# Optimization experiments

Hardware: AMD Instinct MI355X
Metric: run time of the kernel (lower is better)

Reference implementation:

```python
import jax, jax.numpy as jnp
import numpy as np

B, D, V, T = 256, 1024, 32000, 64  # num_seqs, hidden dim, vocab, history len


def setup_inputs() -> dict:
    key = jax.random.key(0)
    ks = jax.random.split(key, 8)
    hidden = jax.random.normal(ks[0], (B, D), dtype=jnp.float32)
    embedding = jax.random.normal(ks[1], (V, D), dtype=jnp.float32) * (1.0 / np.sqrt(D))
    output_tokens = jax.random.randint(ks[2], (B, T), 0, V, dtype=jnp.int64)
    presence_penalties = jax.random.uniform(ks[3], (B,), dtype=jnp.float32)
    frequency_penalties = jax.random.uniform(ks[4], (B,), dtype=jnp.float32)
    temperatures = jax.random.uniform(ks[5], (B,), dtype=jnp.float32) + 0.5  # > eps
    top_ps = jax.random.uniform(ks[6], (B,), dtype=jnp.float32) * 0.5 + 0.5  # in [0.5, 1.0)
    top_ks = jax.random.randint(ks[7], (B,), 1, V, dtype=jnp.int64)
    return {
        "hidden": hidden,
        "embedding": embedding,
        "output_tokens": output_tokens,
        "presence_penalties": presence_penalties,
        "frequency_penalties": frequency_penalties,
        "temperatures": temperatures,
        "top_ps": top_ps,
        "top_ks": top_ks,
    }


def reference(hidden, embedding, output_tokens, presence_penalties,
              frequency_penalties, temperatures, top_ps, top_ks):
    # 1) logits = pruned hidden states @ embedding^T  -> [B, V]
    logits = jnp.einsum("bd,vd->bv", hidden, embedding)
    b, v = logits.shape

    # 2) presence/frequency penalties via per-row token histogram (np.bincount equiv)
    rows = jnp.broadcast_to(jnp.arange(b)[:, None], output_tokens.shape)
    counts = jnp.zeros((b, v), logits.dtype).at[rows, output_tokens].add(1.0)
    logits = logits - frequency_penalties[:, None] * counts \
                    - presence_penalties[:, None] * (counts > 0).astype(logits.dtype)

    # 3) temperature scaling
    logits = logits / temperatures[:, None]

    # 4) probabilities
    probs = jax.nn.softmax(logits, axis=-1)

    # 5) top-p / top-k: descending sort, cumsum masks, scatter back via inverse perm
    order = jnp.argsort(-probs, axis=-1)                       # descending order
    probs_sort = jnp.take_along_axis(probs, order, axis=-1)
    probs_cum = jnp.cumsum(probs_sort, axis=-1)
    top_p_mask = (probs_cum - probs_sort) > top_ps[:, None]
    top_k_mask = jnp.arange(v)[None, :] >= top_ks[:, None]
    probs_sort = jnp.where(top_p_mask | top_k_mask, 0.0, probs_sort)
    inv = jnp.argsort(order, axis=-1)
    filtered_probs = jnp.take_along_axis(probs_sort, inv, axis=-1)  # original order
    return filtered_probs
```

## Files before the change

### kernel.cpp

```cpp
#include <hip/hip_runtime.h>
#include <math.h>

#define NB 256
#define NV 32000
#define ND 1024
#define NT 64

#define GN 64
#define BSTR 40
#define NKB 64
#define AKBF 8192
#define NGBLK (NV / GN)
#define INV2048F 4.8828125e-4f

#define NBIN 1024
#define HSTR 1032
#define HTOT (4 * HSTR)
#define FIX2 4294967296.0
#define SMASK ((1ull << 48) - 1ull)
#define SMEM_BYTES (NV * 4 + HTOT * 4)

typedef _Float16 f16x8 __attribute__((ext_vector_type(8)));
typedef _Float16 f16x4 __attribute__((ext_vector_type(4)));
typedef float f32x16 __attribute__((ext_vector_type(16)));

struct RowP2 {
  unsigned long long basePack;
  unsigned long long toppZfix;
  unsigned pfx;
  int ktop;
  float invZ;
  unsigned ustar;
  int m;
  int cEq;
};

__device__ __forceinline__ unsigned mono_enc(float f) {
  unsigned u = __float_as_uint(f);
  return (u & 0x80000000u) ? ~u : (u | 0x80000000u);
}
__device__ __forceinline__ float mono_dec(unsigned u) {
  return (u & 0x80000000u) ? __uint_as_float(u & 0x7FFFFFFFu) : __uint_as_float(~u);
}

__global__ __launch_bounds__(256) void convert_A(const float* __restrict__ hidden,
                                                 _Float16* __restrict__ A3) {
  const int g = blockIdx.x * 256 + threadIdx.x;
  const int kb = g >> 10, rem = g & 1023, r = rem >> 2, c = rem & 3;
  const float4 a4 = *(const float4*)(hidden + (size_t)r * ND + kb * 16 + c * 4);
  const float v[4] = {a4.x, a4.y, a4.z, a4.w};
  f16x4 h4, q4;
#pragma unroll
  for (int q = 0; q < 4; q++) {
    const _Float16 hh = (_Float16)v[q];
    h4[q] = hh;
    q4[q] = (_Float16)((v[q] - (float)hh) * 2048.0f);
  }
  const int s = r >> 5, l31 = r & 31;
  const int lh = c >> 1, j4 = (c & 1) * 4;
  const int lane = l31 + (lh << 5);
  _Float16* base = A3 + (size_t)kb * AKBF;
  *(f16x4*)(base + ((s * 2 + 0) * 64 + lane) * 8 + j4) = h4;
  *(f16x4*)(base + ((s * 2 + 1) * 64 + lane) * 8 + j4) = q4;
}

__global__ __launch_bounds__(256, 2) void gemm_f16s(
    const float* __restrict__ Bm, const _Float16* __restrict__ A3,
    const float* __restrict__ temp, unsigned* __restrict__ rowmax,
    float* __restrict__ C) {
  __shared__ _Float16 Bls[2][GN * BSTR];
  __shared__ float s_invT[256];
  __shared__ unsigned s_pm[256];

  const int t = threadIdx.x;
  const int l = t & 63, w = t >> 6;
  const int n0 = blockIdx.x * GN;
  s_invT[t] = 1.0f / temp[t];
  s_pm[t] = 0u;

  f32x16 accH[2][2] = {};
  f32x16 accC[2][2] = {};

  const int bn = t >> 2, bk4 = (t & 3) * 4;
  const int l31 = l & 31, lh = l >> 5;
  const int ka = lh * 8;
  const int mb = w * 64;

  const float* browp = Bm + (size_t)(n0 + bn) * ND + bk4;
  const _Float16* aB = A3 + 2048 * w + l * 8;

  f16x8 eh0, eh1, eq0, eq1;
  f16x8 oh0, oh1, oq0, oq1;

#define LOADA(P, KB)                                                  \
  do {                                                                \
    const _Float16* ap_ = aB + (size_t)(KB) * AKBF;                   \
    P##h0 = *(const f16x8*)(ap_);                                     \
    P##q0 = *(const f16x8*)(ap_ + 512);                               \
    P##h1 = *(const f16x8*)(ap_ + 1024);                              \
    P##q1 = *(const f16x8*)(ap_ + 1536);                              \
  } while (0)

#define BCONV(BV, DST)                                                \
  do {                                                                \
    f16x4 h4_, q4_;                                                   \
    const float vv_[4] = {(BV).x, (BV).y, (BV).z, (BV).w};            \
    _Pragma("unroll") for (int j_ = 0; j_ < 4; j_++) {                \
      const _Float16 h_ = (_Float16)vv_[j_];                          \
      h4_[j_] = h_;                                                   \
      q4_[j_] = (_Float16)((vv_[j_] - (float)h_) * 2048.0f);          \
    }                                                                 \
    _Float16* prow_ = (DST) + bn * BSTR;                              \
    *(f16x4*)(prow_ + bk4) = h4_;                                     \
    *(f16x4*)(prow_ + 16 + bk4) = q4_;                                \
  } while (0)

#define COMPUTE(P, CUR)                                                                     \
  do {                                                                                      \
    const _Float16* Bp_ = &Bls[CUR][0] + (size_t)l31 * BSTR + ka;                           \
    f16x8 b0h_ = *(const f16x8*)(Bp_);                                                      \
    f16x8 b1h_ = *(const f16x8*)(Bp_ + 32 * BSTR);                                          \
    accH[0][0] = __builtin_amdgcn_mfma_f32_32x32x16_f16(P##h0, b0h_, accH[0][0], 0, 0, 0);  \
    accH[0][1] = __builtin_amdgcn_mfma_f32_32x32x16_f16(P##h0, b1h_, accH[0][1], 0, 0, 0);  \
    accH[1][0] = __builtin_amdgcn_mfma_f32_32x32x16_f16(P##h1, b0h_, accH[1][0], 0, 0, 0);  \
    accH[1][1] = __builtin_amdgcn_mfma_f32_32x32x16_f16(P##h1, b1h_, accH[1][1], 0, 0, 0);  \
    f16x8 b0q_ = *(const f16x8*)(Bp_ + 16);                                                 \
    f16x8 b1q_ = *(const f16x8*)(Bp_ + 32 * BSTR + 16);                                     \
    accC[0][0] = __builtin_amdgcn_mfma_f32_32x32x16_f16(P##h0, b0q_, accC[0][0], 0, 0, 0);  \
    accC[0][1] = __builtin_amdgcn_mfma_f32_32x32x16_f16(P##h0, b1q_, accC[0][1], 0, 0, 0);  \
    accC[1][0] = __builtin_amdgcn_mfma_f32_32x32x16_f16(P##h1, b0q_, accC[1][0], 0, 0, 0);  \
    accC[1][1] = __builtin_amdgcn_mfma_f32_32x32x16_f16(P##h1, b1q_, accC[1][1], 0, 0, 0);  \
    accC[0][0] = __builtin_amdgcn_mfma_f32_32x32x16_f16(P##q0, b0h_, accC[0][0], 0, 0, 0);  \
    accC[0][1] = __builtin_amdgcn_mfma_f32_32x32x16_f16(P##q0, b1h_, accC[0][1], 0, 0, 0);  \
    accC[1][0] = __builtin_amdgcn_mfma_f32_32x32x16_f16(P##q1, b0h_, accC[1][0], 0, 0, 0);  \
    accC[1][1] = __builtin_amdgcn_mfma_f32_32x32x16_f16(P##q1, b1h_, accC[1][1], 0, 0, 0);  \
  } while (0)

  LOADA(e, 0);
  __builtin_amdgcn_sched_barrier(0);
  float4 bv0 = *(const float4*)(browp);
  __builtin_amdgcn_sched_barrier(0);
  LOADA(o, 1);
  __builtin_amdgcn_sched_barrier(0);
  float4 bvA = *(const float4*)(browp + 16);
  __builtin_amdgcn_sched_barrier(0);
  BCONV(bv0, &Bls[0][0]);
  asm volatile("s_waitcnt lgkmcnt(0)\ns_barrier" ::: "memory");

  float4 bvB;
  for (int kb = 0; kb < 62; kb += 2) {
    COMPUTE(e, 0);
    __builtin_amdgcn_sched_barrier(0);
    LOADA(e, kb + 2);
    __builtin_amdgcn_sched_barrier(0);
    bvB = *(const float4*)(browp + (size_t)(kb + 2) * 16);
    __builtin_amdgcn_sched_barrier(0);
    BCONV(bvA, &Bls[1][0]);
    asm volatile("s_waitcnt lgkmcnt(0)\ns_barrier" ::: "memory");

    COMPUTE(o, 1);
    __builtin_amdgcn_sched_barrier(0);
    LOADA(o, kb + 3);
    __builtin_amdgcn_sched_barrier(0);
    bvA = *(const float4*)(browp + (size_t)(kb + 3) * 16);
    __builtin_amdgcn_sched_barrier(0);
    BCONV(bvB, &Bls[0][0]);
    asm volatile("s_waitcnt lgkmcnt(0)\ns_barrier" ::: "memory");
  }
  COMPUTE(e, 0);
  __builtin_amdgcn_sched_barrier(0);
  BCONV(bvA, &Bls[1][0]);
  asm volatile("s_waitcnt lgkmcnt(0)\ns_barrier" ::: "memory");
  COMPUTE(o, 1);

#undef LOADA
#undef BCONV
#undef COMPUTE

#pragma unroll
  for (int mi = 0; mi < 2; mi++) {
#pragma unroll
    for (int r = 0; r < 16; r++) {
      const int row = mb + mi * 32 + (r & 3) + 8 * (r >> 2) + 4 * lh;
      const float it = s_invT[row];
      float v0 = (accH[mi][0][r] + accC[mi][0][r] * INV2048F) * it;
      float v1 = (accH[mi][1][r] + accC[mi][1][r] * INV2048F) * it;
      C[(size_t)row * NV + n0 + l31] = v0;
      C[(size_t)row * NV + n0 + 32 + l31] = v1;
      float mx = fmaxf(v0, v1);
#pragma unroll
      for (int o = 1; o < 32; o <<= 1) mx = fmaxf(mx, __shfl_xor(mx, o));
      if (l31 == 0) atomicMax(&s_pm[row], mono_enc(mx));
    }
  }
  __syncthreads();
  atomicMax(&rowmax[t], s_pm[t]);
}

__global__ __launch_bounds__(1024) void sample_row(
    float* __restrict__ buf, const unsigned* __restrict__ rowmax,
    const int* __restrict__ toks, const float* __restrict__ pres,
    const float* __restrict__ freq, const float* __restrict__ temp,
    const float* __restrict__ topp_a, const int* __restrict__ topk_a) {
  extern __shared__ char smem[];
  float* e = (float*)smem;
  unsigned* hist = (unsigned*)(smem + NV * 4);
  unsigned long long* suf = (unsigned long long*)hist;
  __shared__ int s_tok[NT];
  __shared__ int s_bs;
  __shared__ RowP2 sp;

  const int b = blockIdx.x, t = threadIdx.x;
  const int cp = (t >> 6) & 1;
  unsigned* loP = hist + cp * HSTR;
  unsigned* hcP = hist + 2 * HSTR + cp * HSTR;
  float* row = buf + (size_t)b * NV;

#define HACC(EV, BIN)                                                    \
  do {                                                                   \
    unsigned long long f_ = (unsigned long long)((double)(EV) * FIX2);   \
    unsigned flo_ = (unsigned)f_;                                        \
    unsigned old_ = atomicAdd(&loP[BIN], flo_);                          \
    unsigned hc_ = 0x10000u + (unsigned)(f_ >> 32) +                     \
                   ((old_ + flo_ < flo_) ? 1u : 0u);                     \
    atomicAdd(&hcP[BIN], hc_);                                           \
  } while (0)

  if (t < NT) s_tok[t] = toks[b * NT + t];
  for (int i = t; i < HTOT; i += 1024) hist[i] = 0u;
  for (int i4 = t; i4 < NV / 4; i4 += 1024)
    *(float4*)(e + i4 * 4) = *(const float4*)(row + i4 * 4);
  __syncthreads();

  if (t < NT) {
    const int tk = s_tok[t];
    bool first = true; int cnt = 0;
    for (int j = 0; j < NT; j++)
      if (s_tok[j] == tk) { if (j < t) first = false; cnt++; }
    if (first) e[tk] -= (freq[b] * (float)cnt + pres[b]) / temp[b];
  }
  __syncthreads();

  const float M = mono_dec(rowmax[b]);
  for (int i4 = t; i4 < NV / 4; i4 += 1024) {
    float4 x4 = *(const float4*)(e + i4 * 4);
    float4 e4;
    e4.x = expf(x4.x - M); e4.y = expf(x4.y - M);
    e4.z = expf(x4.z - M); e4.w = expf(x4.w - M);
    *(float4*)(e + i4 * 4) = e4;
    unsigned k;
    k = __float_as_uint(e4.x); if (k) HACC(e4.x, k >> 20);
    k = __float_as_uint(e4.y); if (k) HACC(e4.y, k >> 20);
    k = __float_as_uint(e4.z); if (k) HACC(e4.z, k >> 20);
    k = __float_as_uint(e4.w); if (k) HACC(e4.w, k >> 20);
  }
  __syncthreads();

  for (int level = 0; level < 3; level++) {
    const unsigned lo0 = hist[t], lo1 = hist[HSTR + t];
    const unsigned hc0 = hist[2 * HSTR + t], hc1 = hist[3 * HSTR + t];
    const unsigned c = (hc0 >> 16) + (hc1 >> 16);
    const unsigned long long sum =
        (((unsigned long long)((hc0 & 0xFFFFu) + (hc1 & 0xFFFFu))) << 32) +
        (unsigned long long)lo0 + (unsigned long long)lo1;
    const unsigned long long v = ((unsigned long long)c << 48) + sum;
    __syncthreads();
    suf[t] = v;
    __syncthreads();
    for (int off = 1; off < NBIN; off <<= 1) {
      unsigned long long add = (t + off < NBIN) ? suf[t + off] : 0ull;
      __syncthreads();
      suf[t] += add;
      __syncthreads();
    }
    const unsigned long long totalP = suf[0];
    if (t == 0) s_bs = NBIN - 1;
    __syncthreads();

    unsigned long long base, toppZ;
    int ktop_;
    if (level == 0) {
      ktop_ = topk_a[b];
      unsigned long long Zfix = totalP & SMASK;
      if (!Zfix) Zfix = 1ull;
      toppZ = (unsigned long long)((double)topp_a[b] * (double)Zfix);
      base = 0ull;
    } else {
      base = sp.basePack; toppZ = sp.toppZfix; ktop_ = sp.ktop;
    }

    {
      const unsigned long long sG = base + suf[t];
      const bool A = ((long long)(sG >> 48) < (long long)ktop_) && ((sG & SMASK) <= toppZ);
      const unsigned long long sP = base + ((t > 0) ? suf[t - 1] : totalP);
      const bool Ap = ((long long)(sP >> 48) < (long long)ktop_) && ((sP & SMASK) <= toppZ);
      if (A && !Ap) s_bs = t;
    }
    __syncthreads();
    if (t == 0) {
      const int bs = s_bs;
      const unsigned long long newBase = base + suf[bs];
      if (level == 0) {
        unsigned long long Zfix = totalP & SMASK;
        if (!Zfix) Zfix = 1ull;
        sp.invZ = (float)(FIX2 / (double)Zfix);
      }
      if (level < 2) {
        sp.basePack = newBase;
        sp.toppZfix = toppZ;
        sp.ktop = ktop_;
        sp.pfx = (level == 0) ? (unsigned)bs : ((sp.pfx << 10) | (unsigned)bs);
      } else {
        const unsigned ustar = (sp.pfx << 10) | (unsigned)bs;
        const unsigned long long raw = ((bs > 0) ? suf[bs - 1] : totalP) - suf[bs];
        const int cEq = (int)(raw >> 48);
        const long long Chi = (long long)(newBase >> 48);
        const unsigned long long Shi = newBase & SMASK;
        long long m = cEq;
        const long long lim = (long long)ktop_ - Chi;
        if (lim < m) m = lim;
        const double tf = (double)__uint_as_float(ustar) * FIX2;
        const double rem = (double)(toppZ - Shi);
        const double Rd = floor(rem / tf) + 1.0;
        if (Rd < (double)m) m = (long long)Rd;
        if (m < 1) m = 1;
        sp.ustar = ustar; sp.m = (int)m; sp.cEq = cEq;
      }
    }
    __syncthreads();

    if (level < 2) {
      for (int i = t; i < HTOT; i += 1024) hist[i] = 0u;
      __syncthreads();
      const unsigned pfx = sp.pfx;
      const int ms = (level == 0) ? 20 : 10;
      const int bsh = (level == 0) ? 10 : 0;
      for (int i4 = t; i4 < NV / 4; i4 += 1024) {
        float4 e4 = *(const float4*)(e + i4 * 4);
        unsigned k;
        k = __float_as_uint(e4.x); if (k && (k >> ms) == pfx) HACC(e4.x, (k >> bsh) & 1023u);
        k = __float_as_uint(e4.y); if (k && (k >> ms) == pfx) HACC(e4.y, (k >> bsh) & 1023u);
        k = __float_as_uint(e4.z); if (k && (k >> ms) == pfx) HACC(e4.z, (k >> bsh) & 1023u);
        k = __float_as_uint(e4.w); if (k && (k >> ms) == pfx) HACC(e4.w, (k >> bsh) & 1023u);
      }
      __syncthreads();
    }
  }
#undef HACC

  const unsigned ustar = sp.ustar;
  const float invZ = sp.invZ;
  if (sp.m >= sp.cEq) {
    for (int i4 = t; i4 < NV / 4; i4 += 1024) {
      float4 e4 = *(const float4*)(e + i4 * 4);
      float4 o4;
      unsigned k;
      k = __float_as_uint(e4.x); o4.x = (k >= ustar) ? e4.x * invZ : 0.f;
      k = __float_as_uint(e4.y); o4.y = (k >= ustar) ? e4.y * invZ : 0.f;
      k = __float_as_uint(e4.z); o4.z = (k >= ustar) ? e4.z * invZ : 0.f;
      k = __float_as_uint(e4.w); o4.w = (k >= ustar) ? e4.w * invZ : 0.f;
      *(float4*)(row + i4 * 4) = o4;
    }
  } else {
    const int m = sp.m;
    unsigned* rk = hist;
    const int base0 = t * 32;
    const int end0 = (base0 + 32 < NV) ? base0 + 32 : NV;
    int myc = 0;
    for (int v = base0; v < end0; v++)
      myc += (__float_as_uint(e[v]) == ustar);
    rk[t] = (unsigned)myc;
    __syncthreads();
    for (int off = 1; off < 1024; off <<= 1) {
      const unsigned a0 = rk[t];
      const unsigned an = (t >= off) ? rk[t - off] : 0u;
      __syncthreads();
      rk[t] = a0 + an;
      __syncthreads();
    }
    int r = (t > 0) ? (int)rk[t - 1] : 0;
    for (int v = base0; v < end0; v++) {
      const unsigned k = __float_as_uint(e[v]);
      float o = (k > ustar) ? e[v] * invZ : 0.f;
      if (k == ustar) { o = (r < m) ? e[v] * invZ : 0.f; r++; }
      row[v] = o;
    }
  }
}

extern "C" void kernel_launch(void* const* d_in, const int* in_sizes, int n_in,
                              void* d_out, int out_size, void* d_ws, size_t ws_size,
                              hipStream_t stream) {
  (void)in_sizes; (void)n_in; (void)out_size; (void)ws_size;
  const float* hidden = (const float*)d_in[0];
  const float* emb    = (const float*)d_in[1];
  const int*   toks   = (const int*)d_in[2];
  const float* pres   = (const float*)d_in[3];
  const float* freq   = (const float*)d_in[4];
  const float* temp   = (const float*)d_in[5];
  const float* topp   = (const float*)d_in[6];
  const int*   topk   = (const int*)d_in[7];
  float* out = (float*)d_out;

  const size_t offA3 = 0;
  const size_t offRM = 1048576;

  _Float16* A3 = (_Float16*)((char*)d_ws + offA3);
  unsigned* rowmax = (unsigned*)((char*)d_ws + offRM);

  hipFuncSetAttribute((const void*)sample_row,
                      hipFuncAttributeMaxDynamicSharedMemorySize, SMEM_BYTES);

  hipMemsetAsync((char*)d_ws + offRM, 0, 1024, stream);
  convert_A<<<256, 256, 0, stream>>>(hidden, A3);
  gemm_f16s<<<NGBLK, 256, 0, stream>>>(emb, A3, temp, rowmax, out);
  sample_row<<<NB, 1024, SMEM_BYTES, stream>>>(out, rowmax, toks, pres, freq,
                                               temp, topp, topk);
}
```

Baseline: 267.4 us.

## Double GEMM k-step per barrier, warp-shuffle suffix scan, integer fixed-point histogram

The GEMM main loop now processes two 16-wide k sub-blocks per pipeline stage. Each stage loads eight A fragments and converts eight B floats per thread, which halves the number of barriers and waitcnt stalls. The sampling kernel's 1024-entry suffix sum switches from a log-step shared-memory scan with many __syncthreads to an intra-wave shuffle scan plus a 16-wave totals pass. The histogram fixed-point conversion also changes from a double multiply to integer mantissa shifts. The cost is more register pressure in the GEMM and possible rounding differences for very small values in the conversion.

```diff
diff --git a/kernel.cpp b/kernel.cpp
--- a/kernel.cpp
+++ b/kernel.cpp
@@ -9,6 +9,7 @@
 #define GN 64
 #define BSTR 40
 #define NKB 64
+#define NK2 32
 #define AKBF 8192
 #define NGBLK (NV / GN)
 #define INV2048F 4.8828125e-4f
@@ -68,7 +69,7 @@
     const float* __restrict__ Bm, const _Float16* __restrict__ A3,
     const float* __restrict__ temp, unsigned* __restrict__ rowmax,
     float* __restrict__ C) {
-  __shared__ _Float16 Bls[2][GN * BSTR];
+  __shared__ _Float16 Bls[2][2][GN * BSTR];
   __shared__ float s_invT[256];
   __shared__ unsigned s_pm[256];
 
@@ -81,101 +82,119 @@
   f32x16 accH[2][2] = {};
   f32x16 accC[2][2] = {};
 
-  const int bn = t >> 2, bk4 = (t & 3) * 4;
+  const int bn = t >> 2, k8 = (t & 3) * 8;
+  const int sub = k8 >> 4, kk = k8 & 15;
   const int l31 = l & 31, lh = l >> 5;
   const int ka = lh * 8;
   const int mb = w * 64;
 
-  const float* browp = Bm + (size_t)(n0 + bn) * ND + bk4;
+  const float* browp = Bm + (size_t)(n0 + bn) * ND + k8;
   const _Float16* aB = A3 + 2048 * w + l * 8;
 
-  f16x8 eh0, eh1, eq0, eq1;
-  f16x8 oh0, oh1, oq0, oq1;
-
-#define LOADA(P, KB)                                                  \
+  f16x8 eh0_0, eq0_0, eh1_0, eq1_0, eh0_1, eq0_1, eh1_1, eq1_1;
+  f16x8 oh0_0, oq0_0, oh1_0, oq1_0, oh0_1, oq0_1, oh1_1, oq1_1;
+
+#define LOADA32(P, KB2)                                               \
   do {                                                                \
-    const _Float16* ap_ = aB + (size_t)(KB) * AKBF;                   \
-    P##h0 = *(const f16x8*)(ap_);                                     \
-    P##q0 = *(const f16x8*)(ap_ + 512);                               \
-    P##h1 = *(const f16x8*)(ap_ + 1024);                              \
-    P##q1 = *(const f16x8*)(ap_ + 1536);                              \
+    const _Float16* a0_ = aB + (size_t)(2 * (KB2)) * AKBF;            \
+    P##h0_0 = *(const f16x8*)(a0_);                                   \
+    P##q0_0 = *(const f16x8*)(a0_ + 512);                             \
+    P##h1_0 = *(const f16x8*)(a0_ + 1024);                            \
+    P##q1_0 = *(const f16x8*)(a0_ + 1536);                            \
+    const _Float16* a1_ = a0_ + AKBF;                                 \
+    P##h0_1 = *(const f16x8*)(a1_);                                   \
+    P##q0_1 = *(const f16x8*)(a1_ + 512);                             \
+    P##h1_1 = *(const f16x8*)(a1_ + 1024);                            \
+    P##q1_1 = *(const f16x8*)(a1_ + 1536);                            \
   } while (0)
 
-#define BCONV(BV, DST)                                                \
+#define BCONV32(V0, V1, BUF)                                          \
   do {                                                                \
-    f16x4 h4_, q4_;                                                   \
-    const float vv_[4] = {(BV).x, (BV).y, (BV).z, (BV).w};            \
-    _Pragma("unroll") for (int j_ = 0; j_ < 4; j_++) {                \
+    const float vv_[8] = {(V0).x, (V0).y, (V0).z, (V0).w,             \
+                          (V1).x, (V1).y, (V1).z, (V1).w};            \
+    f16x8 h8_, q8_;                                                   \
+    _Pragma("unroll") for (int j_ = 0; j_ < 8; j_++) {                \
       const _Float16 h_ = (_Float16)vv_[j_];                          \
-      h4_[j_] = h_;                                                   \
-      q4_[j_] = (_Float16)((vv_[j_] - (float)h_) * 2048.0f);          \
+      h8_[j_] = h_;                                                   \
+      q8_[j_] = (_Float16)((vv_[j_] - (float)h_) * 2048.0f);          \
     }                                                                 \
-    _Float16* prow_ = (DST) + bn * BSTR;                              \
-    *(f16x4*)(prow_ + bk4) = h4_;                                     \
-    *(f16x4*)(prow_ + 16 + bk4) = q4_;                                \
+    _Float16* prow_ = &Bls[BUF][sub][0] + bn * BSTR;                  \
+    *(f16x8*)(prow_ + kk) = h8_;                                      \
+    *(f16x8*)(prow_ + 16 + kk) = q8_;                                 \
   } while (0)
 
-#define COMPUTE(P, CUR)                                                                     \
-  do {                                                                                      \
-    const _Float16* Bp_ = &Bls[CUR][0] + (size_t)l31 * BSTR + ka;                           \
-    f16x8 b0h_ = *(const f16x8*)(Bp_);                                                      \
-    f16x8 b1h_ = *(const f16x8*)(Bp_ + 32 * BSTR);                                          \
-    accH[0][0] = __builtin_amdgcn_mfma_f32_32x32x16_f16(P##h0, b0h_, accH[0][0], 0, 0, 0);  \
-    accH[0][1] = __builtin_amdgcn_mfma_f32_32x32x16_f16(P##h0, b1h_, accH[0][1], 0, 0, 0);  \
-    accH[1][0] = __builtin_amdgcn_mfma_f32_32x32x16_f16(P##h1, b0h_, accH[1][0], 0, 0, 0);  \
-    accH[1][1] = __builtin_amdgcn_mfma_f32_32x32x16_f16(P##h1, b1h_, accH[1][1], 0, 0, 0);  \
-    f16x8 b0q_ = *(const f16x8*)(Bp_ + 16);                                                 \
-    f16x8 b1q_ = *(const f16x8*)(Bp_ + 32 * BSTR + 16);                                     \
-    accC[0][0] = __builtin_amdgcn_mfma_f32_32x32x16_f16(P##h0, b0q_, accC[0][0], 0, 0, 0);  \
-    accC[0][1] = __builtin_amdgcn_mfma_f32_32x32x16_f16(P##h0, b1q_, accC[0][1], 0, 0, 0);  \
-    accC[1][0] = __builtin_amdgcn_mfma_f32_32x32x16_f16(P##h1, b0q_, accC[1][0], 0, 0, 0);  \
-    accC[1][1] = __builtin_amdgcn_mfma_f32_32x32x16_f16(P##h1, b1q_, accC[1][1], 0, 0, 0);  \
-    accC[0][0] = __builtin_amdgcn_mfma_f32_32x32x16_f16(P##q0, b0h_, accC[0][0], 0, 0, 0);  \
-    accC[0][1] = __builtin_amdgcn_mfma_f32_32x32x16_f16(P##q0, b1h_, accC[0][1], 0, 0, 0);  \
-    accC[1][0] = __builtin_amdgcn_mfma_f32_32x32x16_f16(P##q1, b0h_, accC[1][0], 0, 0, 0);  \
-    accC[1][1] = __builtin_amdgcn_mfma_f32_32x32x16_f16(P##q1, b1h_, accC[1][1], 0, 0, 0);  \
+#define CSUB(H0, Q0, H1, Q1, CUR, S)                                                     \
+  do {                                                                                   \
+    const _Float16* Bp_ = &Bls[CUR][S][0] + (size_t)l31 * BSTR + ka;                     \
+    f16x8 b0h_ = *(const f16x8*)(Bp_);                                                   \
+    f16x8 b1h_ = *(const f16x8*)(Bp_ + 32 * BSTR);                                       \
+    accH[0][0] = __builtin_amdgcn_mfma_f32_32x32x16_f16(H0, b0h_, accH[0][0], 0, 0, 0);  \
+    accH[0][1] = __builtin_amdgcn_mfma_f32_32x32x16_f16(H0, b1h_, accH[0][1], 0, 0, 0);  \
+    accH[1][0] = __builtin_amdgcn_mfma_f32_32x32x16_f16(H1, b0h_, accH[1][0], 0, 0, 0);  \
+    accH[1][1] = __builtin_amdgcn_mfma_f32_32x32x16_f16(H1, b1h_, accH[1][1], 0, 0, 0);  \
+    f16x8 b0q_ = *(const f16x8*)(Bp_ + 16);                                              \
+    f16x8 b1q_ = *(const f16x8*)(Bp_ + 32 * BSTR + 16);                                  \
+    accC[0][0] = __builtin_amdgcn_mfma_f32_32x32x16_f16(H0, b0q_, accC[0][0], 0, 0, 0);  \
+    accC[0][1] = __builtin_amdgcn_mfma_f32_32x32x16_f16(H0, b1q_, accC[0][1], 0, 0, 0);  \
+    accC[1][0] = __builtin_amdgcn_mfma_f32_32x32x16_f16(H1, b0q_, accC[1][0], 0, 0, 0);  \
+    accC[1][1] = __builtin_amdgcn_mfma_f32_32x32x16_f16(H1, b1q_, accC[1][1], 0, 0, 0);  \
+    accC[0][0] = __builtin_amdgcn_mfma_f32_32x32x16_f16(Q0, b0h_, accC[0][0], 0, 0, 0);  \
+    accC[0][1] = __builtin_amdgcn_mfma_f32_32x32x16_f16(Q0, b1h_, accC[0][1], 0, 0, 0);  \
+    accC[1][0] = __builtin_amdgcn_mfma_f32_32x32x16_f16(Q1, b0h_, accC[1][0], 0, 0, 0);  \
+    accC[1][1] = __builtin_amdgcn_mfma_f32_32x32x16_f16(Q1, b1h_, accC[1][1], 0, 0, 0);  \
   } while (0)
 
-  LOADA(e, 0);
+#define COMPUTE32(P, CUR)                                             \
+  do {                                                                \
+    CSUB(P##h0_0, P##q0_0, P##h1_0, P##q1_0, CUR, 0);                 \
+    CSUB(P##h0_1, P##q0_1, P##h1_1, P##q1_1, CUR, 1);                 \
+  } while (0)
+
+  LOADA32(e, 0);
   __builtin_amdgcn_sched_barrier(0);
-  float4 bv0 = *(const float4*)(browp);
+  float4 b00 = *(const float4*)(browp);
+  float4 b01 = *(const float4*)(browp + 4);
   __builtin_amdgcn_sched_barrier(0);
-  LOADA(o, 1);
+  LOADA32(o, 1);
   __builtin_amdgcn_sched_barrier(0);
-  float4 bvA = *(const float4*)(browp + 16);
+  float4 bvA0 = *(const float4*)(browp + 32);
+  float4 bvA1 = *(const float4*)(browp + 36);
   __builtin_amdgcn_sched_barrier(0);
-  BCONV(bv0, &Bls[0][0]);
+  BCONV32(b00, b01, 0);
   asm volatile("s_waitcnt lgkmcnt(0)\ns_barrier" ::: "memory");
 
-  float4 bvB;
-  for (int kb = 0; kb < 62; kb += 2) {
-    COMPUTE(e, 0);
-    __builtin_amdgcn_sched_barrier(0);
-    LOADA(e, kb + 2);
-    __builtin_amdgcn_sched_barrier(0);
-    bvB = *(const float4*)(browp + (size_t)(kb + 2) * 16);
-    __builtin_amdgcn_sched_barrier(0);
-    BCONV(bvA, &Bls[1][0]);
+  float4 bvB0, bvB1;
+  for (int kb2 = 0; kb2 < 30; kb2 += 2) {
+    COMPUTE32(e, 0);
+    __builtin_amdgcn_sched_barrier(0);
+    LOADA32(e, kb2 + 2);
+    __builtin_amdgcn_sched_barrier(0);
+    bvB0 = *(const float4*)(browp + (size_t)(kb2 + 2) * 32);
+    bvB1 = *(const float4*)(browp + (size_t)(kb2 + 2) * 32 + 4);
+    __builtin_amdgcn_sched_barrier(0);
+    BCONV32(bvA0, bvA1, 1);
     asm volatile("s_waitcnt lgkmcnt(0)\ns_barrier" ::: "memory");
 
-    COMPUTE(o, 1);
-    __builtin_amdgcn_sched_barrier(0);
-    LOADA(o, kb + 3);
-    __builtin_amdgcn_sched_barrier(0);
-    bvA = *(const float4*)(browp + (size_t)(kb + 3) * 16);
-    __builtin_amdgcn_sched_barrier(0);
-    BCONV(bvB, &Bls[0][0]);
+    COMPUTE32(o, 1);
+    __builtin_amdgcn_sched_barrier(0);
+    LOADA32(o, kb2 + 3);
+    __builtin_amdgcn_sched_barrier(0);
+    bvA0 = *(const float4*)(browp + (size_t)(kb2 + 3) * 32);
+    bvA1 = *(const float4*)(browp + (size_t)(kb2 + 3) * 32 + 4);
+    __builtin_amdgcn_sched_barrier(0);
+    BCONV32(bvB0, bvB1, 0);
     asm volatile("s_waitcnt lgkmcnt(0)\ns_barrier" ::: "memory");
   }
-  COMPUTE(e, 0);
+  COMPUTE32(e, 0);
   __builtin_amdgcn_sched_barrier(0);
-  BCONV(bvA, &Bls[1][0]);
+  BCONV32(bvA0, bvA1, 1);
   asm volatile("s_waitcnt lgkmcnt(0)\ns_barrier" ::: "memory");
-  COMPUTE(o, 1);
-
-#undef LOADA
-#undef BCONV
-#undef COMPUTE
+  COMPUTE32(o, 1);
+
+#undef LOADA32
+#undef BCONV32
+#undef CSUB
+#undef COMPUTE32
 
 #pragma unroll
   for (int mi = 0; mi < 2; mi++) {
@@ -206,6 +225,7 @@
   float* e = (float*)smem;
   unsigned* hist = (unsigned*)(smem + NV * 4);
   unsigned long long* suf = (unsigned long long*)hist;
+  __shared__ unsigned long long wtot16[16];
   __shared__ int s_tok[NT];
   __shared__ int s_bs;
   __shared__ RowP2 sp;
@@ -216,14 +236,17 @@
   unsigned* hcP = hist + 2 * HSTR + cp * HSTR;
   float* row = buf + (size_t)b * NV;
 
-#define HACC(EV, BIN)                                                    \
-  do {                                                                   \
-    unsigned long long f_ = (unsigned long long)((double)(EV) * FIX2);   \
-    unsigned flo_ = (unsigned)f_;                                        \
-    unsigned old_ = atomicAdd(&loP[BIN], flo_);                          \
-    unsigned hc_ = 0x10000u + (unsigned)(f_ >> 32) +                     \
-                   ((old_ + flo_ < flo_) ? 1u : 0u);                     \
-    atomicAdd(&hcP[BIN], hc_);                                           \
+#define HACC(K, BIN)                                                            \
+  do {                                                                          \
+    unsigned long long m_ = (unsigned long long)(((K) & 0x7FFFFFu) | 0x800000u);\
+    const int sh_ = (int)((K) >> 23) - 118;                                     \
+    const unsigned long long f_ =                                               \
+        (sh_ >= 0) ? (m_ << sh_) : ((sh_ > -24) ? (m_ >> (-sh_)) : 0ull);       \
+    const unsigned flo_ = (unsigned)f_;                                         \
+    const unsigned old_ = atomicAdd(&loP[BIN], flo_);                           \
+    const unsigned hc_ = 0x10000u + (unsigned)(f_ >> 32) +                      \
+                         ((old_ + flo_ < flo_) ? 1u : 0u);                      \
+    atomicAdd(&hcP[BIN], hc_);                                                  \
   } while (0)
 
   if (t < NT) s_tok[t] = toks[b * NT + t];
@@ -249,13 +272,14 @@
     e4.z = expf(x4.z - M); e4.w = expf(x4.w - M);
     *(float4*)(e + i4 * 4) = e4;
     unsigned k;
-    k = __float_as_uint(e4.x); if (k) HACC(e4.x, k >> 20);
-    k = __float_as_uint(e4.y); if (k) HACC(e4.y, k >> 20);
-    k = __float_as_uint(e4.z); if (k) HACC(e4.z, k >> 20);
-    k = __float_as_uint(e4.w); if (k) HACC(e4.w, k >> 20);
+    k = __float_as_uint(e4.x); if (k) HACC(k, k >> 20);
+    k = __float_as_uint(e4.y); if (k) HACC(k, k >> 20);
+    k = __float_as_uint(e4.z); if (k) HACC(k, k >> 20);
+    k = __float_as_uint(e4.w); if (k) HACC(k, k >> 20);
   }
   __syncthreads();
 
+  const int lane = t & 63, wv = t >> 6;
   for (int level = 0; level < 3; level++) {
     const unsigned lo0 = hist[t], lo1 = hist[HSTR + t];
     const unsigned hc0 = hist[2 * HSTR + t], hc1 = hist[3 * HSTR + t];
@@ -263,18 +287,25 @@
     const unsigned long long sum =
         (((unsigned long long)((hc0 & 0xFFFFu) + (hc1 & 0xFFFFu))) << 32) +
         (unsigned long long)lo0 + (unsigned long long)lo1;
-    const unsigned long long v = ((unsigned long long)c << 48) + sum;
+    unsigned long long sv = ((unsigned long long)c << 48) + sum;
+#pragma unroll
+    for (int off = 1; off < 64; off <<= 1) {
+      const unsigned long long up = __shfl_down(sv, off, 64);
+      if (lane + off < 64) sv += up;
+    }
+    if (lane == 0) wtot16[wv] = sv;
+    if (t == 0) s_bs = NBIN - 1;
     __syncthreads();
-    suf[t] = v;
-    __syncthreads();
-    for (int off = 1; off < NBIN; off <<= 1) {
-      unsigned long long add = (t + off < NBIN) ? suf[t + off] : 0ull;
-      __syncthreads();
-      suf[t] += add;
-      __syncthreads();
-    }
-    const unsigned long long totalP = suf[0];
-    if (t == 0) s_bs = NBIN - 1;
+    unsigned long long add = 0ull, tot = 0ull;
+#pragma unroll
+    for (int w2 = 0; w2 < 16; w2++) {
+      const unsigned long long x = wtot16[w2];
+      tot += x;
+      add += (w2 > wv) ? x : 0ull;
+    }
+    const unsigned long long mySuf = sv + add;
+    suf[t] = mySuf;
+    const unsigned long long totalP = tot;
     __syncthreads();
 
     unsigned long long base, toppZ;
@@ -290,7 +321,7 @@
     }
 
     {
-      const unsigned long long sG = base + suf[t];
+      const unsigned long long sG = base + mySuf;
       const bool A = ((long long)(sG >> 48) < (long long)ktop_) && ((sG & SMASK) <= toppZ);
       const unsigned long long sP = base + ((t > 0) ? suf[t - 1] : totalP);
       const bool Ap = ((long long)(sP >> 48) < (long long)ktop_) && ((sP & SMASK) <= toppZ);
@@ -338,10 +369,10 @@
       for (int i4 = t; i4 < NV / 4; i4 += 1024) {
         float4 e4 = *(const float4*)(e + i4 * 4);
         unsigned k;
-        k = __float_as_uint(e4.x); if (k && (k >> ms) == pfx) HACC(e4.x, (k >> bsh) & 1023u);
-        k = __float_as_uint(e4.y); if (k && (k >> ms) == pfx) HACC(e4.y, (k >> bsh) & 1023u);
-        k = __float_as_uint(e4.z); if (k && (k >> ms) == pfx) HACC(e4.z, (k >> bsh) & 1023u);
-        k = __float_as_uint(e4.w); if (k && (k >> ms) == pfx) HACC(e4.w, (k >> bsh) & 1023u);
+        k = __float_as_uint(e4.x); if (k && (k >> ms) == pfx) HACC(k, (k >> bsh) & 1023u);
+        k = __float_as_uint(e4.y); if (k && (k >> ms) == pfx) HACC(k, (k >> bsh) & 1023u);
+        k = __float_as_uint(e4.z); if (k && (k >> ms) == pfx) HACC(k, (k >> bsh) & 1023u);
+        k = __float_as_uint(e4.w); if (k && (k >> ms) == pfx) HACC(k, (k >> bsh) & 1023u);
       }
       __syncthreads();
     }
```

Result: slower. 348.6 us (+30.4%).
